# Kernel optimization log

Measured on AMD Instinct MI355X. Metric: run time of the kernel, lower is better.

Reference implementation:

```python
import jax, jax.numpy as jnp
import numpy as np

B, S, D, H = 64, 256, 2048, 16
HD = D // H  # 128
MAXS = 256


def setup_inputs() -> dict:
    key = jax.random.key(0)
    ks = jax.random.split(key, 16)
    sc = 0.02
    inp = {
        "q": jax.random.normal(ks[0], (B, S, D), jnp.float32),
        "k": jax.random.normal(ks[1], (B, S, D), jnp.float32),
        "v": jax.random.normal(ks[2], (B, S, D), jnp.float32),
        "attention_mask": jax.random.randint(ks[3], (B, S), 0, 2, jnp.int32),
        # projection weights, torch Linear convention: y = x @ W.T + b
        "Wq": jax.random.normal(ks[4], (D, D), jnp.float32) * sc,
        "bq": jnp.zeros((D,), jnp.float32),
        "Wk": jax.random.normal(ks[5], (D, D), jnp.float32) * sc,
        "bk": jnp.zeros((D,), jnp.float32),
        "Wv": jax.random.normal(ks[6], (D, D), jnp.float32) * sc,
        "bv": jnp.zeros((D,), jnp.float32),
        "Wo": jax.random.normal(ks[7], (D, D), jnp.float32) * sc,
        "bo": jnp.zeros((D,), jnp.float32),
        # additive per-head bias table (max_sequence_length=256)
        "bias_table": jax.random.normal(ks[8], (H, MAXS, MAXS), jnp.float32) * 0.1,
    }
    return inp


def reference(q, k, v, attention_mask, Wq, bq, Wk, bk, Wv, bv, Wo, bo, bias_table):
    def proj(x, W, b):  # (B,S,D) -> (B,H,S,HD)
        y = x @ W.T + b
        return y.reshape(B, S, H, HD).transpose(0, 2, 1, 3)

    qh = proj(q, Wq, bq)
    kh = proj(k, Wk, bk)
    vh = proj(v, Wv, bv)

    # (B,H,Sq,Sk) scores
    scores = jnp.einsum("bhqd,bhkd->bhqk", qh, kh) / jnp.sqrt(jnp.float32(HD))
    scores = scores + bias_table[None, :, :S, :S]
    # mask: (B,Sk) -> (B,1,1,Sk); masked_fill where mask==0
    neg_inf = jnp.finfo(scores.dtype).min
    scores = jnp.where(attention_mask[:, None, None, :] == 0, neg_inf, scores)
    probs = jax.nn.softmax(scores, axis=-1)  # dropout p=0.0 -> identity
    out = jnp.einsum("bhqk,bhkd->bhqd", probs, vh)
    out = out.transpose(0, 2, 1, 3).reshape(B, S, D)
    return out @ Wo.T + bo
```

## Files before the change

kernel.cpp:

```cpp
#include <hip/hip_runtime.h>
#include <hip/hip_bf16.h>

typedef __attribute__((ext_vector_type(4))) float f32x4;
typedef __attribute__((ext_vector_type(8))) short s16x8;
typedef __attribute__((ext_vector_type(4))) unsigned short u16x4;
typedef __attribute__((ext_vector_type(8))) unsigned short u16x8;
typedef __attribute__((ext_vector_type(4))) int i32x4;

#define NB 64
#define NS 256
#define ND 2048
#define NH 16
#define NHD 128

__device__ __forceinline__ unsigned short f2bf(float f){
  unsigned int u = __float_as_uint(f);
  u += 0x7fffu + ((u >> 16) & 1u);
  return (unsigned short)(u >> 16);
}

__device__ __forceinline__ void gload16(const void* g, void* l){
  __builtin_amdgcn_global_load_lds(
    (const __attribute__((address_space(1))) unsigned int*)g,
    (__attribute__((address_space(3))) unsigned int*)l, 16, 0, 0);
}

#define SBAR()  __builtin_amdgcn_sched_barrier(0)
#define BARRIER() do{ SBAR(); __builtin_amdgcn_s_barrier(); SBAR(); }while(0)
#define WAIT_LGKM0() do{ asm volatile("s_waitcnt lgkmcnt(0)" ::: "memory"); SBAR(); }while(0)
#define WAIT_VM0()   do{ asm volatile("s_waitcnt vmcnt(0)"   ::: "memory"); SBAR(); }while(0)

__global__ __launch_bounds__(256) void wconv(const float* __restrict__ s,
                                             unsigned short* __restrict__ d, int n8){
  int i = blockIdx.x*256 + threadIdx.x;
  if (i >= n8) return;
  f32x4 a = *(const f32x4*)(s + (size_t)i*8);
  f32x4 b = *(const f32x4*)(s + (size_t)i*8 + 4);
  u16x8 u;
  #pragma unroll
  for (int r=0;r<4;r++){ u[r]=f2bf(a[r]); u[4+r]=f2bf(b[r]); }
  *(u16x8*)(d + (size_t)i*8) = u;
}

template<int OUTMODE>
__global__ __launch_bounds__(512, 2) void gemm256(
    const unsigned short* __restrict__ A, const unsigned short* __restrict__ Bw,
    const float* __restrict__ bias, void* __restrict__ Out, int m_base)
{
  extern __shared__ __attribute__((aligned(16))) char ldsb[];
  const int tid  = threadIdx.x;
  const int lane = tid & 63, wid = tid >> 6;
  const int g = lane >> 4, l15 = lane & 15;
  const int wm = wid >> 2, wn = wid & 3;

  const int nwg = gridDim.x, bid = blockIdx.x;
  const int swz = (bid & 7) * (nwg >> 3) + (bid >> 3);
  const int mt = swz >> 3, nt = swz & 7;
  const int m0 = mt*256, n0 = nt*256;

  const int srow_l = tid >> 3;
  const int scol   = (((tid & 7) ^ (srow_l & 7)) * 8);
  const unsigned short* gsrc[4];
  gsrc[0] = A  + (size_t)(m0 +       srow_l)*ND + scol;
  gsrc[1] = A  + (size_t)(m0 + 128 + srow_l)*ND + scol;
  gsrc[2] = Bw + (size_t)(n0 +       srow_l)*ND + scol;
  gsrc[3] = Bw + (size_t)(n0 + 128 + srow_l)*ND + scol;

#define STAGE(buf, p, kt) do{ \
    const unsigned short* s_ = gsrc[p] + (kt); \
    char* d_ = ldsb + (buf)*65536 + ((p)>>1)*32768 + ((p)&1)*16384 + tid*16; \
    gload16(s_, d_); gload16(s_ + (size_t)64*ND, d_ + 8192); }while(0)

#define RD_A(buf, qa) do{ \
    _Pragma("unroll") for (int i_=0;i_<4;i_++){ \
      int hr = (qa)*64 + i_*16 + l15; \
      const char* p_ = ldsb + (buf)*65536 + wm*16384 + hr*128; \
      _Pragma("unroll") for (int ks_=0;ks_<2;ks_++) \
        av[i_][ks_] = *(const s16x8*)(p_ + (((ks_*4+g) ^ (hr&7))*16)); } }while(0)

#define RD_B(buf, dst, qb) do{ \
    _Pragma("unroll") for (int j_=0;j_<2;j_++){ \
      int hc = (wn&1)*64 + (qb)*32 + j_*16 + l15; \
      const char* p_ = ldsb + (buf)*65536 + 32768 + (wn>>1)*16384 + hc*128; \
      _Pragma("unroll") for (int ks_=0;ks_<2;ks_++) \
        dst[j_][ks_] = *(const s16x8*)(p_ + (((ks_*4+g) ^ (hc&7))*16)); } }while(0)

#define MFMA_PH(qa, qb, bv) do{ \
    __builtin_amdgcn_s_setprio(1); \
    _Pragma("unroll") for (int i_=0;i_<4;i_++) \
      _Pragma("unroll") for (int j_=0;j_<2;j_++) \
        _Pragma("unroll") for (int ks_=0;ks_<2;ks_++) \
          acc[(qa)*4+i_][(qb)*2+j_] = __builtin_amdgcn_mfma_f32_16x16x32_bf16( \
              av[i_][ks_], bv[j_][ks_], acc[(qa)*4+i_][(qb)*2+j_], 0,0,0); \
    __builtin_amdgcn_s_setprio(0); }while(0)

  f32x4 acc[8][4];
  s16x8 av[4][2], bva[2][2], bvb[2][2];

  STAGE(0,0,0); STAGE(0,1,0); STAGE(0,2,0); STAGE(0,3,0);
  #pragma unroll
  for (int i=0;i<8;i++)
    #pragma unroll
    for (int j=0;j<4;j++) acc[i][j] = f32x4{0.f,0.f,0.f,0.f};
  WAIT_VM0();
  BARRIER();

  for (int t = 0; t < 16; ++t) {
    const int kt1 = t*128 + 64, kt2 = t*128 + 128;
    RD_A(0,0); RD_B(0,bva,0);
    STAGE(1,0,kt1);
    BARRIER(); WAIT_LGKM0();
    MFMA_PH(0,0,bva);
    BARRIER();
    RD_B(0,bvb,1);
    STAGE(1,1,kt1);
    BARRIER(); WAIT_LGKM0();
    MFMA_PH(0,1,bvb);
    BARRIER();
    RD_A(0,1);
    STAGE(1,2,kt1);
    BARRIER(); WAIT_LGKM0();
    MFMA_PH(1,0,bva);
    BARRIER();
    STAGE(1,3,kt1);
    BARRIER(); WAIT_LGKM0();
    MFMA_PH(1,1,bvb);
    WAIT_VM0();
    BARRIER();
    RD_A(1,0); RD_B(1,bva,0);
    if (t < 15) STAGE(0,0,kt2);
    BARRIER(); WAIT_LGKM0();
    MFMA_PH(0,0,bva);
    BARRIER();
    RD_B(1,bvb,1);
    if (t < 15) STAGE(0,1,kt2);
    BARRIER(); WAIT_LGKM0();
    MFMA_PH(0,1,bvb);
    BARRIER();
    RD_A(1,1);
    if (t < 15) STAGE(0,2,kt2);
    BARRIER(); WAIT_LGKM0();
    MFMA_PH(1,0,bva);
    BARRIER();
    if (t < 15) STAGE(0,3,kt2);
    BARRIER(); WAIT_LGKM0();
    MFMA_PH(1,1,bvb);
    WAIT_VM0();
    BARRIER();
  }

  #pragma unroll
  for (int jx=0;jx<4;jx++){
    int n = n0 + wn*64 + ((jx>>1)<<5) + ((jx&1)<<4) + l15;
    float bj = bias[n];
    #pragma unroll
    for (int i=0;i<8;i++){
      int mb = m_base + m0 + wm*128 + ((i>>2)<<6) + ((i&3)<<4) + g*4;
      if (OUTMODE == 2){
        float* O = (float*)Out;
        #pragma unroll
        for (int r=0;r<4;r++) O[(size_t)(mb+r)*ND + n] = acc[i][jx][r] + bj;
      } else if (OUTMODE == 0){
        unsigned short* O = (unsigned short*)Out;
        int bb = mb >> 8, h = n >> 7, d = n & 127, s0 = mb & 255;
        #pragma unroll
        for (int r=0;r<4;r++)
          O[(((size_t)bb*NH + h)*NS + s0 + r)*NHD + d] = f2bf(acc[i][jx][r] + bj);
      } else {
        unsigned short* O = (unsigned short*)Out;
        int bb = mb >> 8, h = n >> 7, d = n & 127, s0 = mb & 255;
        u16x4 u;
        #pragma unroll
        for (int r=0;r<4;r++) u[r] = f2bf(acc[i][jx][r] + bj);
        *(u16x4*)(O + (((size_t)bb*NH + h)*NHD + d)*NS + s0) = u;
      }
    }
  }
#undef STAGE
#undef RD_A
#undef RD_B
#undef MFMA_PH
}

__global__ __launch_bounds__(256) void attn_fused_kernel(
  const unsigned short* __restrict__ Qh, const unsigned short* __restrict__ Kh,
  const unsigned short* __restrict__ VT, const int* __restrict__ mask,
  const float* __restrict__ bias_table, unsigned short* __restrict__ AO)
{
  __shared__ unsigned short KV[256*128];
  __shared__ unsigned short Plds[4*16*256];
  char* KVb = (char*)KV;
  const int bh = blockIdx.x >> 2, qt = blockIdx.x & 3;
  const int b = bh >> 4, h = bh & 15;
  const int tid = threadIdx.x;
  const int lane = tid & 63, wid = tid >> 6;
  const int g = lane >> 4, l15 = lane & 15;
  const int q = qt*64 + wid*16 + l15;

  {
    const unsigned short* Kb = Kh + (size_t)bh*NS*NHD;
    int srow = tid >> 4, slot = tid & 15;
    #pragma unroll
    for (int c=0;c<16;c++){
      int row = c*16 + srow;
      int ss  = slot ^ (row & 7);
      gload16(Kb + (size_t)row*NHD + ss*8, KVb + c*4096 + tid*16);
    }
  }
  const unsigned short* Qrow = Qh + ((size_t)bh*NS + q)*NHD;
  s16x8 bq[4];
  #pragma unroll
  for (int kk=0;kk<4;kk++) bq[kk] = *(const s16x8*)(Qrow + kk*32 + g*8);

  __syncthreads();

  f32x4 c[16];
  #pragma unroll
  for (int kb=0;kb<16;kb++){
    c[kb] = f32x4{0.f,0.f,0.f,0.f};
    int row = kb*16 + l15;
    #pragma unroll
    for (int kk=0;kk<4;kk++){
      s16x8 a = *(const s16x8*)(KVb + row*256 + (((kk*4+g) ^ (row&7))*16));
      c[kb] = __builtin_amdgcn_mfma_f32_16x16x32_bf16(a, bq[kk], c[kb], 0,0,0);
    }
  }

  const float scale = 0.08838834764831845f;
  const float* brow = bias_table + ((size_t)h*NS + q)*NS;
  const int*   mrow = mask + b*NS;
  float mx = -3.0e38f;
  #pragma unroll
  for (int kb=0;kb<16;kb++){
    f32x4 b4 = *(const f32x4*)(brow + kb*16 + g*4);
    i32x4 m4 = *(const i32x4*)(mrow + kb*16 + g*4);
    #pragma unroll
    for (int r=0;r<4;r++){
      float val = (m4[r] != 0) ? (c[kb][r]*scale + b4[r]) : -3.0e38f;
      c[kb][r] = val;
      mx = fmaxf(mx, val);
    }
  }
  mx = fmaxf(mx, __shfl_xor(mx, 16));
  mx = fmaxf(mx, __shfl_xor(mx, 32));
  float sum = 0.f;
  #pragma unroll
  for (int kb=0;kb<16;kb++)
    #pragma unroll
    for (int r=0;r<4;r++){
      float p = __expf(c[kb][r] - mx);
      c[kb][r] = p; sum += p;
    }
  sum += __shfl_xor(sum, 16);
  sum += __shfl_xor(sum, 32);
  float inv = 1.f / sum;

  {
    char* Pw = (char*)Plds + wid*8192;
    #pragma unroll
    for (int kb=0;kb<16;kb++){
      u16x4 u;
      #pragma unroll
      for (int r=0;r<4;r++) u[r] = f2bf(c[kb][r] * inv);
      *(u16x4*)(Pw + l15*512 + (((2*kb + (g>>1)) ^ (l15&7))*16) + (g&1)*8) = u;
    }
  }

  __syncthreads();

  {
    const unsigned short* Vb = VT + (size_t)bh*NHD*NS;
    int srow = tid >> 5, slot = tid & 31;
    #pragma unroll
    for (int c2=0;c2<16;c2++){
      int row = c2*8 + srow;
      int ss  = slot ^ (row & 7);
      gload16(Vb + (size_t)row*NS + ss*8, KVb + c2*4096 + tid*16);
    }
  }
  __syncthreads();

  const char* Pr = (const char*)Plds + wid*8192;
  #pragma unroll
  for (int dt=0;dt<8;dt++){
    f32x4 acc = f32x4{0.f,0.f,0.f,0.f};
    int row = dt*16 + l15;
    #pragma unroll
    for (int kk=0;kk<8;kk++){
      s16x8 a  = *(const s16x8*)(KVb + row*512 + (((kk*4+g) ^ (row&7))*16));
      s16x8 pb = *(const s16x8*)(Pr  + l15*512 + (((kk*4+g) ^ (l15&7))*16));
      acc = __builtin_amdgcn_mfma_f32_16x16x32_bf16(a, pb, acc, 0,0,0);
    }
    u16x4 u;
    #pragma unroll
    for (int r=0;r<4;r++) u[r] = f2bf(acc[r]);
    *(u16x4*)(AO + ((size_t)b*NS + q)*ND + h*NHD + dt*16 + g*4) = u;
  }
}

extern "C" void kernel_launch(void* const* d_in, const int* in_sizes, int n_in,
                              void* d_out, int out_size, void* d_ws, size_t ws_size,
                              hipStream_t stream)
{
  const float* q  = (const float*)d_in[0];
  const float* k  = (const float*)d_in[1];
  const float* v  = (const float*)d_in[2];
  const int* mask = (const int*)d_in[3];
  const float* Wq = (const float*)d_in[4];
  const float* bq = (const float*)d_in[5];
  const float* Wk = (const float*)d_in[6];
  const float* bk = (const float*)d_in[7];
  const float* Wv = (const float*)d_in[8];
  const float* bv = (const float*)d_in[9];
  const float* Wo = (const float*)d_in[10];
  const float* bo = (const float*)d_in[11];
  const float* bias_table = (const float*)d_in[12];

  char* ws = (char*)d_ws;
  unsigned short* Wob = (unsigned short*)(ws + 0);
  unsigned short* wb  = (unsigned short*)(ws + 8388608);
  unsigned short* tmp = (unsigned short*)(ws + 16777216);
  unsigned short* Qh  = (unsigned short*)(ws + 50331648);
  unsigned short* Kh  = (unsigned short*)(ws + 117440512);
  unsigned short* VT  = (unsigned short*)(ws + 184549376);
  unsigned short* AO  = (unsigned short*)(ws + 251658240);

  hipFuncSetAttribute((const void*)gemm256<0>, hipFuncAttributeMaxDynamicSharedMemorySize, 131072);
  hipFuncSetAttribute((const void*)gemm256<1>, hipFuncAttributeMaxDynamicSharedMemorySize, 131072);
  hipFuncSetAttribute((const void*)gemm256<2>, hipFuncAttributeMaxDynamicSharedMemorySize, 131072);

  wconv<<<2048,256,0,stream>>>(Wo, Wob, 524288);

  const float* acts[3]  = {q, k, v};
  const float* wgt[3]   = {Wq, Wk, Wv};
  const float* bia[3]   = {bq, bk, bv};
  unsigned short* outs[3] = {Qh, Kh, VT};

  for (int x = 0; x < 3; ++x) {
    wconv<<<2048,256,0,stream>>>(wgt[x], wb, 524288);
    for (int hhalf = 0; hhalf < 2; ++hhalf) {
      const float* src = acts[x] + (size_t)hhalf*8192*ND;
      wconv<<<8192,256,0,stream>>>(src, tmp, 2097152);
      if (x < 2)
        gemm256<0><<<256,512,131072,stream>>>(tmp, wb, bia[x], outs[x], hhalf*8192);
      else
        gemm256<1><<<256,512,131072,stream>>>(tmp, wb, bia[x], outs[x], hhalf*8192);
    }
  }

  attn_fused_kernel<<<4096,256,0,stream>>>(Qh,Kh,VT,mask,bias_table,AO);
  gemm256<2><<<512,512,131072,stream>>>(AO,Wob,bo,(float*)d_out,0);
}
```

Measured before the change: 842.2 us.

## Restructure attention to one block per head with K/V resident and register-shuffled P

The attention kernel now runs one 512-thread block per (batch, head) instead of four blocks per head, so K and V are each loaded into LDS once and reused by all query rows. The V load is issued alongside K and overlapped with the QK^T and softmax of the first pass. P is passed to the PV MFMA through lane shuffles instead of an LDS round-trip, and s_setprio is raised around the MFMA loops. Separately, the projection GEMMs now process the whole batch in one launch instead of two halves, with workspace offsets moved to fit the larger temporary buffer. In exchange the larger LDS footprint limits occupancy to one attention block per CU.

Measured after the change: 779.1 us. 1.08x faster.

```diff
diff --git a/kernel.cpp b/kernel.cpp
--- a/kernel.cpp
+++ b/kernel.cpp
@@ -29,6 +29,7 @@
 #define BARRIER() do{ SBAR(); __builtin_amdgcn_s_barrier(); SBAR(); }while(0)
 #define WAIT_LGKM0() do{ asm volatile("s_waitcnt lgkmcnt(0)" ::: "memory"); SBAR(); }while(0)
 #define WAIT_VM0()   do{ asm volatile("s_waitcnt vmcnt(0)"   ::: "memory"); SBAR(); }while(0)
+#define WAIT_VM8()   do{ asm volatile("s_waitcnt vmcnt(8)"   ::: "memory"); SBAR(); }while(0)
 
 __global__ __launch_bounds__(256) void wconv(const float* __restrict__ s,
                                              unsigned short* __restrict__ d, int n8){
@@ -182,120 +183,143 @@
 #undef MFMA_PH
 }
 
-__global__ __launch_bounds__(256) void attn_fused_kernel(
+__global__ __launch_bounds__(512, 1) void attn_fused2(
   const unsigned short* __restrict__ Qh, const unsigned short* __restrict__ Kh,
   const unsigned short* __restrict__ VT, const int* __restrict__ mask,
   const float* __restrict__ bias_table, unsigned short* __restrict__ AO)
 {
-  __shared__ unsigned short KV[256*128];
-  __shared__ unsigned short Plds[4*16*256];
-  char* KVb = (char*)KV;
-  const int bh = blockIdx.x >> 2, qt = blockIdx.x & 3;
-  const int b = bh >> 4, h = bh & 15;
-  const int tid = threadIdx.x;
-  const int lane = tid & 63, wid = tid >> 6;
+  __shared__ unsigned short Klds[256*128];
+  __shared__ unsigned short Vlds[128*256];
+  char* Kb_ = (char*)Klds; char* Vb_ = (char*)Vlds;
+  const int bh = blockIdx.x, b = bh >> 4, h = bh & 15;
+  const int tid = threadIdx.x, lane = tid & 63, w = tid >> 6;
   const int g = lane >> 4, l15 = lane & 15;
-  const int q = qt*64 + wid*16 + l15;
 
   {
-    const unsigned short* Kb = Kh + (size_t)bh*NS*NHD;
-    int srow = tid >> 4, slot = tid & 15;
-    #pragma unroll
-    for (int c=0;c<16;c++){
-      int row = c*16 + srow;
-      int ss  = slot ^ (row & 7);
-      gload16(Kb + (size_t)row*NHD + ss*8, KVb + c*4096 + tid*16);
-    }
-  }
-  const unsigned short* Qrow = Qh + ((size_t)bh*NS + q)*NHD;
-  s16x8 bq[4];
-  #pragma unroll
-  for (int kk=0;kk<4;kk++) bq[kk] = *(const s16x8*)(Qrow + kk*32 + g*8);
-
-  __syncthreads();
-
-  f32x4 c[16];
-  #pragma unroll
-  for (int kb=0;kb<16;kb++){
-    c[kb] = f32x4{0.f,0.f,0.f,0.f};
-    int row = kb*16 + l15;
-    #pragma unroll
-    for (int kk=0;kk<4;kk++){
-      s16x8 a = *(const s16x8*)(KVb + row*256 + (((kk*4+g) ^ (row&7))*16));
-      c[kb] = __builtin_amdgcn_mfma_f32_16x16x32_bf16(a, bq[kk], c[kb], 0,0,0);
-    }
-  }
+    const unsigned short* Ksrc = Kh + (size_t)bh*NS*NHD;
+    int r0 = tid >> 4, sl = tid & 15;
+    #pragma unroll
+    for (int c=0;c<8;c++){
+      int row = c*32 + r0;
+      gload16(Ksrc + (size_t)row*NHD + ((sl ^ (row&7))*8), Kb_ + c*8192 + tid*16);
+    }
+  }
+  {
+    const unsigned short* Vsrc = VT + (size_t)bh*NHD*NS;
+    int r0 = tid >> 5, sl = tid & 31;
+    #pragma unroll
+    for (int c=0;c<8;c++){
+      int row = c*16 + r0;
+      gload16(Vsrc + (size_t)row*NS + ((sl ^ (row&7))*8), Vb_ + c*8192 + tid*16);
+    }
+  }
+  WAIT_VM8();
+  BARRIER();
 
   const float scale = 0.08838834764831845f;
-  const float* brow = bias_table + ((size_t)h*NS + q)*NS;
-  const int*   mrow = mask + b*NS;
-  float mx = -3.0e38f;
-  #pragma unroll
-  for (int kb=0;kb<16;kb++){
-    f32x4 b4 = *(const f32x4*)(brow + kb*16 + g*4);
-    i32x4 m4 = *(const i32x4*)(mrow + kb*16 + g*4);
-    #pragma unroll
-    for (int r=0;r<4;r++){
-      float val = (m4[r] != 0) ? (c[kb][r]*scale + b4[r]) : -3.0e38f;
-      c[kb][r] = val;
-      mx = fmaxf(mx, val);
-    }
-  }
-  mx = fmaxf(mx, __shfl_xor(mx, 16));
-  mx = fmaxf(mx, __shfl_xor(mx, 32));
-  float sum = 0.f;
-  #pragma unroll
-  for (int kb=0;kb<16;kb++)
-    #pragma unroll
-    for (int r=0;r<4;r++){
-      float p = __expf(c[kb][r] - mx);
-      c[kb][r] = p; sum += p;
-    }
-  sum += __shfl_xor(sum, 16);
-  sum += __shfl_xor(sum, 32);
-  float inv = 1.f / sum;
-
-  {
-    char* Pw = (char*)Plds + wid*8192;
+  const int* mrow = mask + b*NS;
+  const int s0l = l15 + ((g&1)<<5), s1l = s0l + 16;
+  const int sel = g >> 1;
+
+  auto pass = [&](int p, bool wait_v){
+    const int q = w*32 + p*16 + l15;
+    const unsigned short* Qrow = Qh + ((size_t)bh*NS + q)*NHD;
+    s16x8 bq[4];
+    #pragma unroll
+    for (int kk=0;kk<4;kk++) bq[kk] = *(const s16x8*)(Qrow + kk*32 + g*8);
+
+    f32x4 c[16];
+    __builtin_amdgcn_s_setprio(1);
     #pragma unroll
     for (int kb=0;kb<16;kb++){
+      c[kb] = f32x4{0.f,0.f,0.f,0.f};
+      int row = kb*16 + l15;
+      #pragma unroll
+      for (int kk=0;kk<4;kk++){
+        s16x8 a = *(const s16x8*)(Kb_ + row*256 + (((kk*4+g) ^ (row&7))*16));
+        c[kb] = __builtin_amdgcn_mfma_f32_16x16x32_bf16(a, bq[kk], c[kb], 0,0,0);
+      }
+    }
+    __builtin_amdgcn_s_setprio(0);
+
+    const float* brow = bias_table + ((size_t)h*NS + q)*NS;
+    float mx = -3.0e38f;
+    #pragma unroll
+    for (int kb=0;kb<16;kb++){
+      f32x4 b4 = *(const f32x4*)(brow + kb*16 + g*4);
+      i32x4 m4 = *(const i32x4*)(mrow + kb*16 + g*4);
+      #pragma unroll
+      for (int r=0;r<4;r++){
+        float val = (m4[r] != 0) ? (c[kb][r]*scale + b4[r]) : -3.0e38f;
+        c[kb][r] = val;
+        mx = fmaxf(mx, val);
+      }
+    }
+    mx = fmaxf(mx, __shfl_xor(mx, 16));
+    mx = fmaxf(mx, __shfl_xor(mx, 32));
+    float sum = 0.f;
+    #pragma unroll
+    for (int kb=0;kb<16;kb++)
+      #pragma unroll
+      for (int r=0;r<4;r++){
+        float pv = __expf(c[kb][r] - mx);
+        c[kb][r] = pv; sum += pv;
+      }
+    sum += __shfl_xor(sum, 16);
+    sum += __shfl_xor(sum, 32);
+    float inv = 1.f / sum;
+
+    unsigned int pk[16][2];
+    #pragma unroll
+    for (int kb=0;kb<16;kb++){
+      pk[kb][0] = (unsigned int)f2bf(c[kb][0]*inv) | ((unsigned int)f2bf(c[kb][1]*inv) << 16);
+      pk[kb][1] = (unsigned int)f2bf(c[kb][2]*inv) | ((unsigned int)f2bf(c[kb][3]*inv) << 16);
+    }
+
+    if (wait_v){ WAIT_VM0(); BARRIER(); }
+
+    s16x8 pb[8];
+    #pragma unroll
+    for (int kk=0;kk<8;kk++){
+      unsigned int e0 = (unsigned int)__shfl((int)pk[2*kk][0],   s0l);
+      unsigned int e1 = (unsigned int)__shfl((int)pk[2*kk][1],   s0l);
+      unsigned int e2 = (unsigned int)__shfl((int)pk[2*kk][0],   s1l);
+      unsigned int e3 = (unsigned int)__shfl((int)pk[2*kk][1],   s1l);
+      unsigned int o0 = (unsigned int)__shfl((int)pk[2*kk+1][0], s0l);
+      unsigned int o1 = (unsigned int)__shfl((int)pk[2*kk+1][1], s0l);
+      unsigned int o2 = (unsigned int)__shfl((int)pk[2*kk+1][0], s1l);
+      unsigned int o3 = (unsigned int)__shfl((int)pk[2*kk+1][1], s1l);
+      union { unsigned int wd[4]; s16x8 v; } u_;
+      u_.wd[0] = sel ? o0 : e0; u_.wd[1] = sel ? o1 : e1;
+      u_.wd[2] = sel ? o2 : e2; u_.wd[3] = sel ? o3 : e3;
+      pb[kk] = u_.v;
+    }
+
+    f32x4 oacc[8];
+    __builtin_amdgcn_s_setprio(1);
+    #pragma unroll
+    for (int dt=0;dt<8;dt++){
+      oacc[dt] = f32x4{0.f,0.f,0.f,0.f};
+      int row = dt*16 + l15;
+      #pragma unroll
+      for (int kk=0;kk<8;kk++){
+        s16x8 a = *(const s16x8*)(Vb_ + row*512 + (((kk*4+g) ^ (row&7))*16));
+        oacc[dt] = __builtin_amdgcn_mfma_f32_16x16x32_bf16(a, pb[kk], oacc[dt], 0,0,0);
+      }
+    }
+    __builtin_amdgcn_s_setprio(0);
+
+    #pragma unroll
+    for (int dt=0;dt<8;dt++){
       u16x4 u;
       #pragma unroll
-      for (int r=0;r<4;r++) u[r] = f2bf(c[kb][r] * inv);
-      *(u16x4*)(Pw + l15*512 + (((2*kb + (g>>1)) ^ (l15&7))*16) + (g&1)*8) = u;
-    }
-  }
-
-  __syncthreads();
-
-  {
-    const unsigned short* Vb = VT + (size_t)bh*NHD*NS;
-    int srow = tid >> 5, slot = tid & 31;
-    #pragma unroll
-    for (int c2=0;c2<16;c2++){
-      int row = c2*8 + srow;
-      int ss  = slot ^ (row & 7);
-      gload16(Vb + (size_t)row*NS + ss*8, KVb + c2*4096 + tid*16);
-    }
-  }
-  __syncthreads();
-
-  const char* Pr = (const char*)Plds + wid*8192;
-  #pragma unroll
-  for (int dt=0;dt<8;dt++){
-    f32x4 acc = f32x4{0.f,0.f,0.f,0.f};
-    int row = dt*16 + l15;
-    #pragma unroll
-    for (int kk=0;kk<8;kk++){
-      s16x8 a  = *(const s16x8*)(KVb + row*512 + (((kk*4+g) ^ (row&7))*16));
-      s16x8 pb = *(const s16x8*)(Pr  + l15*512 + (((kk*4+g) ^ (l15&7))*16));
-      acc = __builtin_amdgcn_mfma_f32_16x16x32_bf16(a, pb, acc, 0,0,0);
-    }
-    u16x4 u;
-    #pragma unroll
-    for (int r=0;r<4;r++) u[r] = f2bf(acc[r]);
-    *(u16x4*)(AO + ((size_t)b*NS + q)*ND + h*NHD + dt*16 + g*4) = u;
-  }
+      for (int r=0;r<4;r++) u[r] = f2bf(oacc[dt][r]);
+      *(u16x4*)(AO + ((size_t)b*NS + q)*ND + h*NHD + dt*16 + g*4) = u;
+    }
+  };
+
+  pass(0, true);
+  pass(1, false);
 }
 
 extern "C" void kernel_launch(void* const* d_in, const int* in_sizes, int n_in,
@@ -320,10 +344,10 @@
   unsigned short* Wob = (unsigned short*)(ws + 0);
   unsigned short* wb  = (unsigned short*)(ws + 8388608);
   unsigned short* tmp = (unsigned short*)(ws + 16777216);
-  unsigned short* Qh  = (unsigned short*)(ws + 50331648);
-  unsigned short* Kh  = (unsigned short*)(ws + 117440512);
-  unsigned short* VT  = (unsigned short*)(ws + 184549376);
-  unsigned short* AO  = (unsigned short*)(ws + 251658240);
+  unsigned short* Qh  = (unsigned short*)(ws + 83886080);
+  unsigned short* Kh  = (unsigned short*)(ws + 150994944);
+  unsigned short* VT  = (unsigned short*)(ws + 218103808);
+  unsigned short* AO  = (unsigned short*)(ws + 285212672);
 
   hipFuncSetAttribute((const void*)gemm256<0>, hipFuncAttributeMaxDynamicSharedMemorySize, 131072);
   hipFuncSetAttribute((const void*)gemm256<1>, hipFuncAttributeMaxDynamicSharedMemorySize, 131072);
@@ -338,16 +362,13 @@
 
   for (int x = 0; x < 3; ++x) {
     wconv<<<2048,256,0,stream>>>(wgt[x], wb, 524288);
-    for (int hhalf = 0; hhalf < 2; ++hhalf) {
-      const float* src = acts[x] + (size_t)hhalf*8192*ND;
-      wconv<<<8192,256,0,stream>>>(src, tmp, 2097152);
-      if (x < 2)
-        gemm256<0><<<256,512,131072,stream>>>(tmp, wb, bia[x], outs[x], hhalf*8192);
-      else
-        gemm256<1><<<256,512,131072,stream>>>(tmp, wb, bia[x], outs[x], hhalf*8192);
-    }
-  }
-
-  attn_fused_kernel<<<4096,256,0,stream>>>(Qh,Kh,VT,mask,bias_table,AO);
+    wconv<<<16384,256,0,stream>>>(acts[x], tmp, 4194304);
+    if (x < 2)
+      gemm256<0><<<512,512,131072,stream>>>(tmp, wb, bia[x], outs[x], 0);
+    else
+      gemm256<1><<<512,512,131072,stream>>>(tmp, wb, bia[x], outs[x], 0);
+  }
+
+  attn_fused2<<<1024,512,0,stream>>>(Qh,Kh,VT,mask,bias_table,AO);
   gemm256<2><<<512,512,131072,stream>>>(AO,Wob,bo,(float*)d_out,0);
 }
```
